# Performance work log

Hardware: AMD Instinct MI355X
Metric: run time of the kernel (lower is better)

Reference implementation:

```python
import jax, jax.numpy as jnp
import numpy as np

NUM_USER = 200000
NUM_ITEM = 200000
DIM_E = 64
DIM_FEAT = 128
B = 16384
NUM_NEG = 16
TEMP = 0.2
LR_LAMBDA = 0.5
NUM_SAMPLE = 0.5


def _l2norm(x, eps=1e-12):
    # F.normalize(x, dim=1): x / max(||x||_2, eps)
    n = jnp.sqrt(jnp.sum(x * x, axis=1, keepdims=True))
    return x / jnp.maximum(n, eps)


def setup_inputs() -> dict:
    key = jax.random.key(0)
    ks = jax.random.split(key, 9)
    G = 1 + NUM_NEG
    N = B * G
    v_feat = jax.random.normal(ks[0], (NUM_ITEM, DIM_FEAT), dtype=jnp.float32)
    id_embedding = jax.random.normal(ks[1], (NUM_USER + NUM_ITEM, DIM_E), dtype=jnp.float32) * 0.05
    W1 = jax.random.normal(ks[2], (DIM_FEAT, 256), dtype=jnp.float32) * (1.0 / np.sqrt(DIM_FEAT))
    b1 = jnp.zeros((256,), dtype=jnp.float32)
    W2 = jax.random.normal(ks[3], (256, DIM_E), dtype=jnp.float32) * (1.0 / np.sqrt(256.0))
    b2 = jnp.zeros((DIM_E,), dtype=jnp.float32)
    user_tensor = jax.random.randint(ks[4], (B, G), 0, NUM_USER, dtype=jnp.int32)
    # item ids are global ids in [num_user, num_user + num_item)
    item_tensor = jax.random.randint(ks[5], (B, G), NUM_USER, NUM_USER + NUM_ITEM, dtype=jnp.int32)
    num_to_replace = int(N * NUM_SAMPLE)
    rand_index = jax.random.randint(ks[6], (num_to_replace,), 0, N, dtype=jnp.int32)
    return {
        'v_feat': v_feat, 'id_embedding': id_embedding,
        'W1': W1, 'b1': b1, 'W2': W2, 'b2': b2,
        'user_tensor': user_tensor, 'item_tensor': item_tensor,
        'rand_index': rand_index,
    }


def _encoder(v_feat, W1, b1, W2, b2):
    vf = _l2norm(v_feat)                      # F.normalize in __init__
    h = jax.nn.leaky_relu(vf @ W1 + b1)       # negative_slope=0.01 (torch default)
    return h @ W2 + b2                        # [num_item, dim_E]


def _loss_contrastive(anchor, allv):
    # exp(<a, v>/T) reshaped to [B, 1+num_neg]; col 0 is positive
    s = jnp.exp(jnp.sum(anchor * allv, axis=1) / TEMP).reshape(-1, 1 + NUM_NEG)
    pos = s[:, 0]
    tot = jnp.sum(s, axis=1)
    return jnp.mean(-jnp.log(pos / (tot + 1e-8) + 1e-8))


def reference(v_feat, id_embedding, W1, b1, W2, b2, user_tensor, item_tensor, rand_index):
    G = 1 + NUM_NEG
    feature = _encoder(v_feat, W1, b1, W2, b2)           # [num_item, dim_E]
    pos_item = jnp.repeat(item_tensor[:, :1], G, axis=1).reshape(-1)  # [B*G]
    uflat = user_tensor.reshape(-1)
    iflat = item_tensor.reshape(-1)
    item_idx = jnp.clip(iflat - NUM_USER, 0, feature.shape[0] - 1)
    all_item_feat = feature[item_idx]                    # [B*G, dim_E]
    user_emb = id_embedding[uflat]
    pos_emb = id_embedding[pos_item]
    all_emb = id_embedding[iflat]
    head_feat = _l2norm(all_item_feat)
    head_embed = _l2norm(pos_emb)
    # replace a random subset of embedding rows with encoded features
    all_item_input = all_emb.at[rand_index].set(all_item_feat[rand_index])
    l1 = _loss_contrastive(head_embed, head_feat)
    l2 = _loss_contrastive(user_emb, all_item_input)
    return LR_LAMBDA * l1 + (1.0 - LR_LAMBDA) * l2
```

## Files before the change

kernel.cpp:

```cpp
#include <hip/hip_runtime.h>
#include <hip/hip_bf16.h>

typedef __bf16 bf16_t;
typedef __bf16 bf16x8 __attribute__((ext_vector_type(8)));
typedef __bf16 bf16x4 __attribute__((ext_vector_type(4)));
typedef float f32x4 __attribute__((ext_vector_type(4)));

#define NUM_USER 200000
#define NUM_ITEM 200000
#define DIM_E 64
#define DIM_FEAT 128
#define HID 256
#define BATCH 16384
#define GG 17
#define NN (BATCH * GG)
#define NREP 139264
#define HP 40

__global__ __launch_bounds__(256) void prep2_kernel(
    const float* __restrict__ W1, const float* __restrict__ W2,
    const int* __restrict__ rand_index,
    bf16_t* __restrict__ W1t, bf16_t* __restrict__ W2t,
    unsigned char* __restrict__ mask)
{
    const int t = blockIdx.x * 256 + threadIdx.x;
    if (t < HID * DIM_FEAT) {
        const int n = t >> 7, k = t & 127;
        W1t[t] = (bf16_t)W1[k * HID + n];
    }
    if (t < DIM_E * HID) {
        const int n = t >> 8, k = t & 255;
        W2t[t] = (bf16_t)W2[k * DIM_E + n];
    }
    if (t < NREP) mask[rand_index[t]] = 1;
}

__global__ __launch_bounds__(256, 2) void encoder3_kernel(
    const float* __restrict__ vfeat,
    const bf16_t* __restrict__ W1t, const float* __restrict__ b1v,
    const bf16_t* __restrict__ W2t, const float* __restrict__ b2v,
    float* __restrict__ feature)
{
    const int wave = threadIdx.x >> 6;
    const int lane = threadIdx.x & 63;
    const int m    = lane & 15;
    const int quad = lane >> 4;
    const int wid  = blockIdx.x * 4 + wave;

    __shared__ bf16_t hlds[4][64 * HP];

    if (wid >= 3125) return;
    const size_t row_base = (size_t)wid * 64;
    bf16_t* hw = hlds[wave];

    bf16x8 af[4][4];
#pragma unroll
    for (int s = 0; s < 4; ++s) {
        const size_t row = row_base + s * 16 + m;
        const float* rp = vfeat + row * DIM_FEAT + quad * 8;
        float4 v0[4], v1[4];
#pragma unroll
        for (int ks = 0; ks < 4; ++ks) {
            v0[ks] = *reinterpret_cast<const float4*>(rp + ks * 32);
            v1[ks] = *reinterpret_cast<const float4*>(rp + ks * 32 + 4);
        }
        float ss = 0.f;
#pragma unroll
        for (int ks = 0; ks < 4; ++ks) {
            ss += v0[ks].x * v0[ks].x + v0[ks].y * v0[ks].y
                + v0[ks].z * v0[ks].z + v0[ks].w * v0[ks].w;
            ss += v1[ks].x * v1[ks].x + v1[ks].y * v1[ks].y
                + v1[ks].z * v1[ks].z + v1[ks].w * v1[ks].w;
        }
        ss += __shfl_xor(ss, 16, 64);
        ss += __shfl_xor(ss, 32, 64);
        const float inv = 1.0f / fmaxf(sqrtf(ss), 1e-12f);
#pragma unroll
        for (int ks = 0; ks < 4; ++ks) {
            bf16x8 v;
            v[0] = (bf16_t)(v0[ks].x * inv); v[1] = (bf16_t)(v0[ks].y * inv);
            v[2] = (bf16_t)(v0[ks].z * inv); v[3] = (bf16_t)(v0[ks].w * inv);
            v[4] = (bf16_t)(v1[ks].x * inv); v[5] = (bf16_t)(v1[ks].y * inv);
            v[6] = (bf16_t)(v1[ks].z * inv); v[7] = (bf16_t)(v1[ks].w * inv);
            af[s][ks] = v;
        }
    }

    f32x4 acc2[4][4];
#pragma unroll
    for (int s = 0; s < 4; ++s)
#pragma unroll
        for (int n2 = 0; n2 < 4; ++n2) acc2[s][n2] = (f32x4){0.f, 0.f, 0.f, 0.f};

#pragma unroll
    for (int p = 0; p < 8; ++p) {
#pragma unroll
        for (int h = 0; h < 2; ++h) {
            const int nt = p * 2 + h;
            const bf16_t* bp = W1t + (nt * 16 + m) * DIM_FEAT + quad * 8;
            bf16x8 bfr[4];
#pragma unroll
            for (int ks = 0; ks < 4; ++ks)
                bfr[ks] = *reinterpret_cast<const bf16x8*>(bp + ks * 32);
            const float4 bias1 = *reinterpret_cast<const float4*>(b1v + nt * 16 + quad * 4);
#pragma unroll
            for (int s = 0; s < 4; ++s) {
                f32x4 a1 = (f32x4){0.f, 0.f, 0.f, 0.f};
#pragma unroll
                for (int ks = 0; ks < 4; ++ks)
                    a1 = __builtin_amdgcn_mfma_f32_16x16x32_bf16(bfr[ks], af[s][ks], a1, 0, 0, 0);
                bf16x4 hv4;
#pragma unroll
                for (int i = 0; i < 4; ++i) {
                    float hv = a1[i] + ((const float*)&bias1)[i];
                    hv = hv >= 0.f ? hv : 0.01f * hv;
                    hv4[i] = (bf16_t)hv;
                }
                *reinterpret_cast<bf16x4*>(hw + (s * 16 + m) * HP + h * 16 + quad * 4) = hv4;
            }
        }
        bf16x8 b2f[4];
#pragma unroll
        for (int n2 = 0; n2 < 4; ++n2)
            b2f[n2] = *reinterpret_cast<const bf16x8*>(W2t + (n2 * 16 + m) * HID + p * 32 + quad * 8);
#pragma unroll
        for (int s = 0; s < 4; ++s) {
            const bf16x8 a2 = *reinterpret_cast<const bf16x8*>(hw + (s * 16 + m) * HP + quad * 8);
#pragma unroll
            for (int n2 = 0; n2 < 4; ++n2)
                acc2[s][n2] = __builtin_amdgcn_mfma_f32_16x16x32_bf16(b2f[n2], a2, acc2[s][n2], 0, 0, 0);
        }
    }

#pragma unroll
    for (int n2 = 0; n2 < 4; ++n2) {
        const float4 bias2 = *reinterpret_cast<const float4*>(b2v + n2 * 16 + quad * 4);
#pragma unroll
        for (int s = 0; s < 4; ++s) {
            float4 o;
            o.x = acc2[s][n2][0] + bias2.x;
            o.y = acc2[s][n2][1] + bias2.y;
            o.z = acc2[s][n2][2] + bias2.z;
            o.w = acc2[s][n2][3] + bias2.w;
            *reinterpret_cast<float4*>(
                feature + (row_base + s * 16 + m) * DIM_E + n2 * 16 + quad * 4) = o;
        }
    }
}

__global__ __launch_bounds__(256) void loss_elem2_kernel(
    const float* __restrict__ feature, const float* __restrict__ id_emb,
    const int* __restrict__ user_t, const int* __restrict__ item_t,
    const unsigned char* __restrict__ mask,
    float* __restrict__ s1, float* __restrict__ s2)
{
    const int kq = threadIdx.x & 3;
    const int n  = blockIdx.x * 64 + (threadIdx.x >> 2);
    const int b  = n / GG;
    const int u   = user_t[n];
    const int it  = item_t[n];
    const int pos = item_t[b * GG];
    int fidx = it - NUM_USER;
    fidx = min(max(fidx, 0), NUM_ITEM - 1);

    const float4* fp  = reinterpret_cast<const float4*>(feature + (size_t)fidx * DIM_E) + kq * 4;
    const float4* up  = reinterpret_cast<const float4*>(id_emb + (size_t)u   * DIM_E) + kq * 4;
    const float4* pp  = reinterpret_cast<const float4*>(id_emb + (size_t)pos * DIM_E) + kq * 4;
    const float4* ap  = mask[n] ? fp
                      : reinterpret_cast<const float4*>(id_emb + (size_t)it * DIM_E) + kq * 4;

    float x = 0.f, y = 0.f, z = 0.f, w = 0.f;
#pragma unroll
    for (int j = 0; j < 4; ++j) {
        const float4 f = fp[j];
        const float4 p = pp[j];
        const float4 uu = up[j];
        const float4 a = ap[j];
        x += f.x * f.x + f.y * f.y + f.z * f.z + f.w * f.w;
        y += p.x * p.x + p.y * p.y + p.z * p.z + p.w * p.w;
        z += p.x * f.x + p.y * f.y + p.z * f.z + p.w * f.w;
        w += uu.x * a.x + uu.y * a.y + uu.z * a.z + uu.w * a.w;
    }
#pragma unroll
    for (int off = 1; off <= 2; off <<= 1) {
        x += __shfl_xor(x, off, 64);
        y += __shfl_xor(y, off, 64);
        z += __shfl_xor(z, off, 64);
        w += __shfl_xor(w, off, 64);
    }
    if (kq == 0) {
        const float dot1 = z / (fmaxf(sqrtf(x), 1e-12f) * fmaxf(sqrtf(y), 1e-12f));
        s1[n] = __expf(dot1 * 5.0f);
        s2[n] = __expf(w * 5.0f);
    }
}

__global__ __launch_bounds__(256) void loss_reduce_kernel(
    const float* __restrict__ s1, const float* __restrict__ s2,
    float* __restrict__ partials)
{
    const int b = blockIdx.x * 256 + threadIdx.x;
    float tot1 = 0.f, tot2 = 0.f, p1 = 0.f, p2 = 0.f;
#pragma unroll
    for (int g = 0; g < GG; ++g) {
        const float a1 = s1[b * GG + g];
        const float a2 = s2[b * GG + g];
        if (g == 0) { p1 = a1; p2 = a2; }
        tot1 += a1; tot2 += a2;
    }
    const float l1 = -logf(p1 / (tot1 + 1e-8f) + 1e-8f);
    const float l2 = -logf(p2 / (tot2 + 1e-8f) + 1e-8f);
    float v = 0.5f * l1 + 0.5f * l2;
#pragma unroll
    for (int off = 32; off > 0; off >>= 1) v += __shfl_xor(v, off, 64);
    __shared__ float red[4];
    const int wave = threadIdx.x >> 6, lane = threadIdx.x & 63;
    if (lane == 0) red[wave] = v;
    __syncthreads();
    if (threadIdx.x == 0) partials[blockIdx.x] = red[0] + red[1] + red[2] + red[3];
}

__global__ __launch_bounds__(64) void final_kernel(
    const float* __restrict__ partials, float* __restrict__ out)
{
    float v = partials[threadIdx.x];
#pragma unroll
    for (int off = 32; off > 0; off >>= 1) v += __shfl_xor(v, off, 64);
    if (threadIdx.x == 0) out[0] = v * (1.0f / BATCH);
}

extern "C" void kernel_launch(void* const* d_in, const int* in_sizes, int n_in,
                              void* d_out, int out_size, void* d_ws, size_t ws_size,
                              hipStream_t stream)
{
    (void)in_sizes; (void)n_in; (void)out_size; (void)ws_size;
    const float* v_feat    = (const float*)d_in[0];
    const float* id_emb    = (const float*)d_in[1];
    const float* W1        = (const float*)d_in[2];
    const float* b1        = (const float*)d_in[3];
    const float* W2        = (const float*)d_in[4];
    const float* b2        = (const float*)d_in[5];
    const int*   user_t    = (const int*)d_in[6];
    const int*   item_t    = (const int*)d_in[7];
    const int*   rand_idx  = (const int*)d_in[8];

    char* ws = (char*)d_ws;
    bf16_t*        W1t      = (bf16_t*)(ws + 0);
    bf16_t*        W2t      = (bf16_t*)(ws + 65536);
    unsigned char* mask     = (unsigned char*)(ws + 98304);
    float*         s1       = (float*)(ws + 376832);
    float*         s2       = (float*)(ws + 1490944);
    float*         partials = (float*)(ws + 2605056);
    float*         feature  = (float*)(ws + 2605312);

    hipMemsetAsync(mask, 0, NN, stream);
    prep2_kernel<<<544, 256, 0, stream>>>(W1, W2, rand_idx, W1t, W2t, mask);
    encoder3_kernel<<<782, 256, 0, stream>>>(v_feat, W1t, b1, W2t, b2, feature);
    loss_elem2_kernel<<<4352, 256, 0, stream>>>(feature, id_emb, user_t, item_t, mask, s1, s2);
    loss_reduce_kernel<<<64, 256, 0, stream>>>(s1, s2, partials);
    final_kernel<<<1, 64, 0, stream>>>(partials, (float*)d_out);
}
```

Baseline: 311.9 us.

## Store encoder output in bf16, pass hidden via shuffles, merge final reduce

The encoder now handles 32 rows per wave instead of 64, with a higher occupancy hint. It passes the hidden-layer fragments between lanes with cross-lane shuffles instead of LDS and writes the feature table as bf16. The loss kernel reads the bf16 features, has each thread handle two elements, and always loads the id embedding instead of branching on the mask. The final kernel is dropped in favour of an atomicAdd into a zeroed output. This cuts encoder write and gather traffic and one launch, at the cost of extra bf16 rounding on the feature table and a non-deterministic summation order.

Measured after the change: 330.1 us. 5.8% more time.

```diff
diff --git a/kernel.cpp b/kernel.cpp
--- a/kernel.cpp
+++ b/kernel.cpp
@@ -5,6 +5,7 @@
 typedef __bf16 bf16x8 __attribute__((ext_vector_type(8)));
 typedef __bf16 bf16x4 __attribute__((ext_vector_type(4)));
 typedef float f32x4 __attribute__((ext_vector_type(4)));
+typedef unsigned int u32;
 
 #define NUM_USER 200000
 #define NUM_ITEM 200000
@@ -15,7 +16,6 @@
 #define GG 17
 #define NN (BATCH * GG)
 #define NREP 139264
-#define HP 40
 
 __global__ __launch_bounds__(256) void prep2_kernel(
     const float* __restrict__ W1, const float* __restrict__ W2,
@@ -35,29 +35,23 @@
     if (t < NREP) mask[rand_index[t]] = 1;
 }
 
-__global__ __launch_bounds__(256, 2) void encoder3_kernel(
+__global__ __launch_bounds__(256, 4) void encoder5_kernel(
     const float* __restrict__ vfeat,
     const bf16_t* __restrict__ W1t, const float* __restrict__ b1v,
     const bf16_t* __restrict__ W2t, const float* __restrict__ b2v,
-    float* __restrict__ feature)
-{
-    const int wave = threadIdx.x >> 6;
+    bf16_t* __restrict__ featB)
+{
     const int lane = threadIdx.x & 63;
-    const int m    = lane & 15;
-    const int quad = lane >> 4;
-    const int wid  = blockIdx.x * 4 + wave;
-
-    __shared__ bf16_t hlds[4][64 * HP];
-
-    if (wid >= 3125) return;
-    const size_t row_base = (size_t)wid * 64;
-    bf16_t* hw = hlds[wave];
-
-    bf16x8 af[4][4];
-#pragma unroll
-    for (int s = 0; s < 4; ++s) {
-        const size_t row = row_base + s * 16 + m;
-        const float* rp = vfeat + row * DIM_FEAT + quad * 8;
+    const int r    = lane & 15;
+    const int Q    = lane >> 4;
+    const int wid  = blockIdx.x * 4 + (threadIdx.x >> 6);
+    if (wid >= 6250) return;
+    const size_t row0 = (size_t)wid * 32;
+
+    bf16x8 af[2][4];
+#pragma unroll
+    for (int s = 0; s < 2; ++s) {
+        const float* rp = vfeat + (row0 + s * 16 + r) * DIM_FEAT + Q * 8;
         float4 v0[4], v1[4];
 #pragma unroll
         for (int ks = 0; ks < 4; ++ks) {
@@ -86,29 +80,34 @@
         }
     }
 
-    f32x4 acc2[4][4];
-#pragma unroll
-    for (int s = 0; s < 4; ++s)
+    f32x4 acc2[2][4];
+#pragma unroll
+    for (int s = 0; s < 2; ++s)
 #pragma unroll
         for (int n2 = 0; n2 < 4; ++n2) acc2[s][n2] = (f32x4){0.f, 0.f, 0.f, 0.f};
 
-#pragma unroll
-    for (int p = 0; p < 8; ++p) {
+    const int sl0 = (lane & 15) | ((lane & 16) << 1);
+    const int sl1 = sl0 + 16;
+    const bool hiQ = (Q >= 2);
+
+#pragma unroll
+    for (int t = 0; t < 8; ++t) {
+        u32 pk[2][2][2];
 #pragma unroll
         for (int h = 0; h < 2; ++h) {
-            const int nt = p * 2 + h;
-            const bf16_t* bp = W1t + (nt * 16 + m) * DIM_FEAT + quad * 8;
-            bf16x8 bfr[4];
+            const int nt = t * 2 + h;
+            const bf16_t* bp = W1t + (nt * 16 + r) * DIM_FEAT + Q * 8;
+            bf16x8 w1f[4];
 #pragma unroll
             for (int ks = 0; ks < 4; ++ks)
-                bfr[ks] = *reinterpret_cast<const bf16x8*>(bp + ks * 32);
-            const float4 bias1 = *reinterpret_cast<const float4*>(b1v + nt * 16 + quad * 4);
-#pragma unroll
-            for (int s = 0; s < 4; ++s) {
+                w1f[ks] = *reinterpret_cast<const bf16x8*>(bp + ks * 32);
+            const float4 bias1 = *reinterpret_cast<const float4*>(b1v + nt * 16 + Q * 4);
+#pragma unroll
+            for (int s = 0; s < 2; ++s) {
                 f32x4 a1 = (f32x4){0.f, 0.f, 0.f, 0.f};
 #pragma unroll
                 for (int ks = 0; ks < 4; ++ks)
-                    a1 = __builtin_amdgcn_mfma_f32_16x16x32_bf16(bfr[ks], af[s][ks], a1, 0, 0, 0);
+                    a1 = __builtin_amdgcn_mfma_f32_16x16x32_bf16(w1f[ks], af[s][ks], a1, 0, 0, 0);
                 bf16x4 hv4;
 #pragma unroll
                 for (int i = 0; i < 4; ++i) {
@@ -116,88 +115,119 @@
                     hv = hv >= 0.f ? hv : 0.01f * hv;
                     hv4[i] = (bf16_t)hv;
                 }
-                *reinterpret_cast<bf16x4*>(hw + (s * 16 + m) * HP + h * 16 + quad * 4) = hv4;
+                const uint2 u = __builtin_bit_cast(uint2, hv4);
+                pk[s][h][0] = u.x;
+                pk[s][h][1] = u.y;
             }
         }
-        bf16x8 b2f[4];
+        bf16x8 w2f[4];
 #pragma unroll
         for (int n2 = 0; n2 < 4; ++n2)
-            b2f[n2] = *reinterpret_cast<const bf16x8*>(W2t + (n2 * 16 + m) * HID + p * 32 + quad * 8);
-#pragma unroll
-        for (int s = 0; s < 4; ++s) {
-            const bf16x8 a2 = *reinterpret_cast<const bf16x8*>(hw + (s * 16 + m) * HP + quad * 8);
+            w2f[n2] = *reinterpret_cast<const bf16x8*>(
+                W2t + (n2 * 16 + r) * HID + t * 32 + Q * 8);
+#pragma unroll
+        for (int s = 0; s < 2; ++s) {
+            const u32 q0a = (u32)__shfl((int)pk[s][0][0], sl0, 64);
+            const u32 q0b = (u32)__shfl((int)pk[s][1][0], sl0, 64);
+            const u32 q1a = (u32)__shfl((int)pk[s][0][1], sl0, 64);
+            const u32 q1b = (u32)__shfl((int)pk[s][1][1], sl0, 64);
+            const u32 q2a = (u32)__shfl((int)pk[s][0][0], sl1, 64);
+            const u32 q2b = (u32)__shfl((int)pk[s][1][0], sl1, 64);
+            const u32 q3a = (u32)__shfl((int)pk[s][0][1], sl1, 64);
+            const u32 q3b = (u32)__shfl((int)pk[s][1][1], sl1, 64);
+            uint4 bu;
+            bu.x = hiQ ? q0b : q0a;
+            bu.y = hiQ ? q1b : q1a;
+            bu.z = hiQ ? q2b : q2a;
+            bu.w = hiQ ? q3b : q3a;
+            const bf16x8 hfrag = __builtin_bit_cast(bf16x8, bu);
 #pragma unroll
             for (int n2 = 0; n2 < 4; ++n2)
-                acc2[s][n2] = __builtin_amdgcn_mfma_f32_16x16x32_bf16(b2f[n2], a2, acc2[s][n2], 0, 0, 0);
+                acc2[s][n2] = __builtin_amdgcn_mfma_f32_16x16x32_bf16(w2f[n2], hfrag, acc2[s][n2], 0, 0, 0);
         }
     }
 
 #pragma unroll
     for (int n2 = 0; n2 < 4; ++n2) {
-        const float4 bias2 = *reinterpret_cast<const float4*>(b2v + n2 * 16 + quad * 4);
-#pragma unroll
-        for (int s = 0; s < 4; ++s) {
-            float4 o;
-            o.x = acc2[s][n2][0] + bias2.x;
-            o.y = acc2[s][n2][1] + bias2.y;
-            o.z = acc2[s][n2][2] + bias2.z;
-            o.w = acc2[s][n2][3] + bias2.w;
-            *reinterpret_cast<float4*>(
-                feature + (row_base + s * 16 + m) * DIM_E + n2 * 16 + quad * 4) = o;
-        }
-    }
-}
-
-__global__ __launch_bounds__(256) void loss_elem2_kernel(
-    const float* __restrict__ feature, const float* __restrict__ id_emb,
+        const float4 bias2 = *reinterpret_cast<const float4*>(b2v + n2 * 16 + Q * 4);
+#pragma unroll
+        for (int s = 0; s < 2; ++s) {
+            bf16x4 o;
+            o[0] = (bf16_t)(acc2[s][n2][0] + bias2.x);
+            o[1] = (bf16_t)(acc2[s][n2][1] + bias2.y);
+            o[2] = (bf16_t)(acc2[s][n2][2] + bias2.z);
+            o[3] = (bf16_t)(acc2[s][n2][3] + bias2.w);
+            *reinterpret_cast<bf16x4*>(
+                featB + (row0 + s * 16 + r) * DIM_E + n2 * 16 + Q * 4) = o;
+        }
+    }
+}
+
+__global__ __launch_bounds__(256) void loss_elem4_kernel(
+    const bf16_t* __restrict__ featB, const float* __restrict__ id_emb,
     const int* __restrict__ user_t, const int* __restrict__ item_t,
     const unsigned char* __restrict__ mask,
     float* __restrict__ s1, float* __restrict__ s2)
 {
     const int kq = threadIdx.x & 3;
-    const int n  = blockIdx.x * 64 + (threadIdx.x >> 2);
-    const int b  = n / GG;
-    const int u   = user_t[n];
-    const int it  = item_t[n];
-    const int pos = item_t[b * GG];
-    int fidx = it - NUM_USER;
-    fidx = min(max(fidx, 0), NUM_ITEM - 1);
-
-    const float4* fp  = reinterpret_cast<const float4*>(feature + (size_t)fidx * DIM_E) + kq * 4;
-    const float4* up  = reinterpret_cast<const float4*>(id_emb + (size_t)u   * DIM_E) + kq * 4;
-    const float4* pp  = reinterpret_cast<const float4*>(id_emb + (size_t)pos * DIM_E) + kq * 4;
-    const float4* ap  = mask[n] ? fp
-                      : reinterpret_cast<const float4*>(id_emb + (size_t)it * DIM_E) + kq * 4;
-
-    float x = 0.f, y = 0.f, z = 0.f, w = 0.f;
-#pragma unroll
-    for (int j = 0; j < 4; ++j) {
-        const float4 f = fp[j];
-        const float4 p = pp[j];
-        const float4 uu = up[j];
-        const float4 a = ap[j];
-        x += f.x * f.x + f.y * f.y + f.z * f.z + f.w * f.w;
-        y += p.x * p.x + p.y * p.y + p.z * p.z + p.w * p.w;
-        z += p.x * f.x + p.y * f.y + p.z * f.z + p.w * f.w;
-        w += uu.x * a.x + uu.y * a.y + uu.z * a.z + uu.w * a.w;
-    }
-#pragma unroll
-    for (int off = 1; off <= 2; off <<= 1) {
-        x += __shfl_xor(x, off, 64);
-        y += __shfl_xor(y, off, 64);
-        z += __shfl_xor(z, off, 64);
-        w += __shfl_xor(w, off, 64);
-    }
-    if (kq == 0) {
-        const float dot1 = z / (fmaxf(sqrtf(x), 1e-12f) * fmaxf(sqrtf(y), 1e-12f));
-        s1[n] = __expf(dot1 * 5.0f);
-        s2[n] = __expf(w * 5.0f);
+    const int c  = blockIdx.x * 64 + (threadIdx.x >> 2);
+
+#pragma unroll
+    for (int half = 0; half < 2; ++half) {
+        const int nn = c + half * (NN / 2);
+        const int b  = nn / GG;
+        const int u  = user_t[nn];
+        const int it = item_t[nn];
+        const int pos = item_t[b * GG];
+        int fidx = min(max(it - NUM_USER, 0), NUM_ITEM - 1);
+        const bool rep = mask[nn] != 0;
+
+        const bf16x8* fp = reinterpret_cast<const bf16x8*>(featB + (size_t)fidx * DIM_E + kq * 16);
+        const float4* pp = reinterpret_cast<const float4*>(id_emb + (size_t)pos * DIM_E) + kq * 4;
+        const float4* up = reinterpret_cast<const float4*>(id_emb + (size_t)u   * DIM_E) + kq * 4;
+        const float4* ip = reinterpret_cast<const float4*>(id_emb + (size_t)it  * DIM_E) + kq * 4;
+
+        const bf16x8 f8a = fp[0];
+        const bf16x8 f8b = fp[1];
+
+        float x = 0.f, y = 0.f, z = 0.f, w = 0.f;
+#pragma unroll
+        for (int j = 0; j < 4; ++j) {
+            const float4 p  = pp[j];
+            const float4 uu = up[j];
+            const float4 iv = ip[j];
+            const bf16x8 fb = (j < 2) ? f8a : f8b;
+            float f0 = (float)fb[(j & 1) * 4 + 0];
+            float f1 = (float)fb[(j & 1) * 4 + 1];
+            float f2 = (float)fb[(j & 1) * 4 + 2];
+            float f3 = (float)fb[(j & 1) * 4 + 3];
+            const float a0 = rep ? f0 : iv.x;
+            const float a1 = rep ? f1 : iv.y;
+            const float a2 = rep ? f2 : iv.z;
+            const float a3 = rep ? f3 : iv.w;
+            x += f0 * f0 + f1 * f1 + f2 * f2 + f3 * f3;
+            y += p.x * p.x + p.y * p.y + p.z * p.z + p.w * p.w;
+            z += p.x * f0 + p.y * f1 + p.z * f2 + p.w * f3;
+            w += uu.x * a0 + uu.y * a1 + uu.z * a2 + uu.w * a3;
+        }
+#pragma unroll
+        for (int off = 1; off <= 2; off <<= 1) {
+            x += __shfl_xor(x, off, 64);
+            y += __shfl_xor(y, off, 64);
+            z += __shfl_xor(z, off, 64);
+            w += __shfl_xor(w, off, 64);
+        }
+        if (kq == 0) {
+            const float dot1 = z / (fmaxf(sqrtf(x), 1e-12f) * fmaxf(sqrtf(y), 1e-12f));
+            s1[nn] = __expf(dot1 * 5.0f);
+            s2[nn] = __expf(w * 5.0f);
+        }
     }
 }
 
 __global__ __launch_bounds__(256) void loss_reduce_kernel(
     const float* __restrict__ s1, const float* __restrict__ s2,
-    float* __restrict__ partials)
+    float* __restrict__ out)
 {
     const int b = blockIdx.x * 256 + threadIdx.x;
     float tot1 = 0.f, tot2 = 0.f, p1 = 0.f, p2 = 0.f;
@@ -217,16 +247,8 @@
     const int wave = threadIdx.x >> 6, lane = threadIdx.x & 63;
     if (lane == 0) red[wave] = v;
     __syncthreads();
-    if (threadIdx.x == 0) partials[blockIdx.x] = red[0] + red[1] + red[2] + red[3];
-}
-
-__global__ __launch_bounds__(64) void final_kernel(
-    const float* __restrict__ partials, float* __restrict__ out)
-{
-    float v = partials[threadIdx.x];
-#pragma unroll
-    for (int off = 32; off > 0; off >>= 1) v += __shfl_xor(v, off, 64);
-    if (threadIdx.x == 0) out[0] = v * (1.0f / BATCH);
+    if (threadIdx.x == 0)
+        atomicAdd(out, (red[0] + red[1] + red[2] + red[3]) * (1.0f / BATCH));
 }
 
 extern "C" void kernel_launch(void* const* d_in, const int* in_sizes, int n_in,
@@ -250,13 +272,12 @@
     unsigned char* mask     = (unsigned char*)(ws + 98304);
     float*         s1       = (float*)(ws + 376832);
     float*         s2       = (float*)(ws + 1490944);
-    float*         partials = (float*)(ws + 2605056);
-    float*         feature  = (float*)(ws + 2605312);
+    bf16_t*        featB    = (bf16_t*)(ws + 2605056);
 
     hipMemsetAsync(mask, 0, NN, stream);
+    hipMemsetAsync(d_out, 0, sizeof(float), stream);
     prep2_kernel<<<544, 256, 0, stream>>>(W1, W2, rand_idx, W1t, W2t, mask);
-    encoder3_kernel<<<782, 256, 0, stream>>>(v_feat, W1t, b1, W2t, b2, feature);
-    loss_elem2_kernel<<<4352, 256, 0, stream>>>(feature, id_emb, user_t, item_t, mask, s1, s2);
-    loss_reduce_kernel<<<64, 256, 0, stream>>>(s1, s2, partials);
-    final_kernel<<<1, 64, 0, stream>>>(partials, (float*)d_out);
-}
+    encoder5_kernel<<<1563, 256, 0, stream>>>(v_feat, W1t, b1, W2t, b2, featB);
+    loss_elem4_kernel<<<2176, 256, 0, stream>>>(featB, id_emb, user_t, item_t, mask, s1, s2);
+    loss_reduce_kernel<<<64, 256, 0, stream>>>(s1, s2, (float*)d_out);
+}
```
